# Optimization experiments

Measured on AMD Instinct MI355X. Metric: run time of the kernel, lower is better.

## Reference

```python
import jax, jax.numpy as jnp
import numpy as np

D_MODEL = 1024
N_HEADS = 16
HEAD_DIM = D_MODEL // N_HEADS
D_FF = 4 * D_MODEL
LN_EPS = 1e-5


def setup_inputs() -> dict:
    key = jax.random.key(0)
    ks = jax.random.split(key, 12)
    B, T = 16, 512
    s = lambda fan_in: 1.0 / np.sqrt(fan_in)
    inp = {
        'x': jax.random.normal(ks[0], (B, T, D_MODEL), jnp.float32),
        # torch Linear layout: [out_features, in_features]
        'w_qkv': jax.random.normal(ks[1], (3 * D_MODEL, D_MODEL), jnp.float32) * s(D_MODEL),
        'w_proj': jax.random.normal(ks[2], (D_MODEL, D_MODEL), jnp.float32) * s(D_MODEL),
        'w_ff1': jax.random.normal(ks[3], (D_FF, D_MODEL), jnp.float32) * s(D_MODEL),
        'b_ff1': jax.random.normal(ks[4], (D_FF,), jnp.float32) * 0.02,
        'w_ff2': jax.random.normal(ks[5], (D_MODEL, D_FF), jnp.float32) * s(D_FF),
        'b_ff2': jax.random.normal(ks[6], (D_MODEL,), jnp.float32) * 0.02,
        'ln1_g': jnp.ones((D_MODEL,), jnp.float32),
        'ln1_b': jnp.zeros((D_MODEL,), jnp.float32),
        'ln2_g': jnp.ones((D_MODEL,), jnp.float32),
        'ln2_b': jnp.zeros((D_MODEL,), jnp.float32),
    }
    return inp


def _layernorm(x, g, b):
    mu = jnp.mean(x, axis=-1, keepdims=True)
    var = jnp.var(x, axis=-1, keepdims=True)
    return (x - mu) * jax.lax.rsqrt(var + LN_EPS) * g + b


def _block(x, w_qkv, w_proj, w_ff1, b_ff1, w_ff2, b_ff2, ln1_g, ln1_b, ln2_g, ln2_b):
    B, T, _ = x.shape
    a = _layernorm(x, ln1_g, ln1_b)
    qkv = a @ w_qkv.T  # [B,T,3D]
    q, k, v = jnp.split(qkv, 3, axis=-1)
    # [B,H,T,hd]
    rs = lambda t: t.reshape(B, T, N_HEADS, HEAD_DIM).transpose(0, 2, 1, 3)
    q, k, v = rs(q), rs(k), rs(v)
    scale = HEAD_DIM ** -0.5
    att = jnp.einsum('bhqd,bhkd->bhqk', q, k) * scale
    causal = jnp.tril(jnp.ones((T, T), bool))
    att = jnp.where(causal, att, jnp.float32(-10000.0))
    att = jax.nn.softmax(att, axis=-1)
    out = jnp.einsum('bhqk,bhkd->bhqd', att, v)
    out = out.transpose(0, 2, 1, 3).reshape(B, T, D_MODEL)
    x = x + out @ w_proj.T
    f = _layernorm(x, ln2_g, ln2_b)
    f = jax.nn.gelu(f @ w_ff1.T + b_ff1, approximate=False) @ w_ff2.T + b_ff2
    return x + f


def reference(x, w_qkv, w_proj, w_ff1, b_ff1, w_ff2, b_ff2, ln1_g, ln1_b, ln2_g, ln2_b):
    return _block(x, w_qkv, w_proj, w_ff1, b_ff1, w_ff2, b_ff2, ln1_g, ln1_b, ln2_g, ln2_b)
```

## Files before the change

### kernel.cpp

```cpp
#include <hip/hip_runtime.h>
#include <stdint.h>

typedef __bf16 bf16x8_t __attribute__((ext_vector_type(8)));
typedef float f32x4_t __attribute__((ext_vector_type(4)));
typedef unsigned short ushort8_t __attribute__((ext_vector_type(8)));

#define DEV __device__ __forceinline__

DEV unsigned short f2bf(float f) {
  union { float f; uint32_t u; } v; v.f = f;
  uint32_t r = v.u + 0x7FFFu + ((v.u >> 16) & 1u);
  return (unsigned short)(r >> 16);
}

DEV void gl_lds16(const void* g, void* l) {
  __builtin_amdgcn_global_load_lds(
      (const __attribute__((address_space(1))) void*)g,
      (__attribute__((address_space(3))) void*)l, 16, 0, 0);
}

DEV float gelu_f(float x) {
  const float y = x * 0.7071067811865475f;
  const float ay = fabsf(y);
  const float t = __builtin_amdgcn_rcpf(1.0f + 0.3275911f * ay);
  float p = fmaf(t, 1.061405429f, -1.453152027f);
  p = fmaf(t, p, 1.421413741f);
  p = fmaf(t, p, -0.284496736f);
  p = fmaf(t, p, 0.254829592f);
  p *= t;
  const float e = __expf(-ay * ay);
  float erfv = 1.0f - p * e;
  erfv = copysignf(erfv, y);
  return 0.5f * x * (1.0f + erfv);
}

__global__ __launch_bounds__(256) void cvt_all(const float* __restrict__ w0, unsigned short* __restrict__ o0,
                                               const float* __restrict__ w1, unsigned short* __restrict__ o1,
                                               const float* __restrict__ w2, unsigned short* __restrict__ o2,
                                               const float* __restrict__ w3, unsigned short* __restrict__ o3) {
  int i = blockIdx.x * 256 + threadIdx.x;
  const float* in; unsigned short* outp;
  if (i < 786432) { in = w0; outp = o0; }
  else if (i < 1048576) { in = w1; outp = o1; i -= 786432; }
  else if (i < 2097152) { in = w2; outp = o2; i -= 1048576; }
  else { in = w3; outp = o3; i -= 2097152; }
  float4 v = ((const float4*)in)[i];
  ushort4 o;
  o.x = f2bf(v.x); o.y = f2bf(v.y); o.z = f2bf(v.z); o.w = f2bf(v.w);
  ((ushort4*)outp)[i] = o;
}

__global__ __launch_bounds__(256) void ln_kernel(const float* __restrict__ x,
                                                 const float* __restrict__ g,
                                                 const float* __restrict__ b,
                                                 unsigned short* __restrict__ outp) {
  const int row = blockIdx.x * 4 + (threadIdx.x >> 6);
  const int lane = threadIdx.x & 63;
  const float4* xr = (const float4*)(x + (size_t)row * 1024);
  float4 v[4];
  float s = 0.f, s2 = 0.f;
#pragma unroll
  for (int j = 0; j < 4; ++j) {
    v[j] = xr[j * 64 + lane];
    s += v[j].x + v[j].y + v[j].z + v[j].w;
    s2 += v[j].x * v[j].x + v[j].y * v[j].y + v[j].z * v[j].z + v[j].w * v[j].w;
  }
#pragma unroll
  for (int off = 1; off < 64; off <<= 1) {
    s += __shfl_xor(s, off, 64);
    s2 += __shfl_xor(s2, off, 64);
  }
  const float mu = s * (1.0f / 1024.0f);
  const float var = s2 * (1.0f / 1024.0f) - mu * mu;
  const float rstd = rsqrtf(var + 1e-5f);
  ushort4* orow = (ushort4*)(outp + (size_t)row * 1024);
  const float4* gp = (const float4*)g;
  const float4* bp = (const float4*)b;
#pragma unroll
  for (int j = 0; j < 4; ++j) {
    float4 gv = gp[j * 64 + lane], bv = bp[j * 64 + lane];
    ushort4 o;
    o.x = f2bf((v[j].x - mu) * rstd * gv.x + bv.x);
    o.y = f2bf((v[j].y - mu) * rstd * gv.y + bv.y);
    o.z = f2bf((v[j].z - mu) * rstd * gv.z + bv.z);
    o.w = f2bf((v[j].w - mu) * rstd * gv.w + bv.w);
    orow[j * 64 + lane] = o;
  }
}

template <int MODE>
__global__ __launch_bounds__(256) void gemm_bt(const unsigned short* __restrict__ A,
                                               const unsigned short* __restrict__ B,
                                               float* __restrict__ Cf,
                                               unsigned short* __restrict__ Cb,
                                               const float* __restrict__ bias,
                                               const float* __restrict__ res,
                                               unsigned short* __restrict__ Vt,
                                               int M, int N, int K) {
  __shared__ unsigned short sA[128 * 64];
  __shared__ unsigned short sB[128 * 64];
  const int tid = threadIdx.x;
  const int w = tid >> 6, lane = tid & 63;
  const int kg = lane >> 4, l16 = lane & 15;
  const int wm = (w & 1) * 64, wn = (w >> 1) * 64;
  const int rowBase = blockIdx.y * 128, colBase = blockIdx.x * 128;

  const int sr = tid >> 3;
  const int scc = ((tid & 7) ^ (sr & 7)) * 8;
  const unsigned short* gA = A + (size_t)(rowBase + sr) * K + scc;
  const unsigned short* gB = B + (size_t)(colBase + sr) * K + scc;
  unsigned short* lA = sA + tid * 8;
  unsigned short* lB = sB + tid * 8;

  f32x4_t acc[4][4];
#pragma unroll
  for (int mi = 0; mi < 4; ++mi)
#pragma unroll
    for (int ni = 0; ni < 4; ++ni) acc[mi][ni] = (f32x4_t)0.0f;

  const unsigned short* pA[2][4];
  const unsigned short* pB[2][4];
#pragma unroll
  for (int kd = 0; kd < 2; ++kd)
#pragma unroll
    for (int i = 0; i < 4; ++i) {
      const int kc = kd * 4 + kg;
      pA[kd][i] = sA + (wm + i * 16 + l16) * 64 + ((kc ^ (l16 & 7)) * 8);
      pB[kd][i] = sB + (wn + i * 16 + l16) * 64 + ((kc ^ (l16 & 7)) * 8);
    }

  const int nk = K >> 6;
  for (int kt = 0; kt < nk; ++kt) {
    __syncthreads();
#pragma unroll
    for (int i = 0; i < 4; ++i) {
      gl_lds16(gA + (size_t)(32 * i) * K, lA + 2048 * i);
      gl_lds16(gB + (size_t)(32 * i) * K, lB + 2048 * i);
    }
    gA += 64; gB += 64;
    __syncthreads();
#pragma unroll
    for (int kd = 0; kd < 2; ++kd) {
      bf16x8_t a[4], b[4];
#pragma unroll
      for (int i = 0; i < 4; ++i) a[i] = *(const bf16x8_t*)pA[kd][i];
#pragma unroll
      for (int i = 0; i < 4; ++i) b[i] = *(const bf16x8_t*)pB[kd][i];
#pragma unroll
      for (int mi = 0; mi < 4; ++mi)
#pragma unroll
        for (int ni = 0; ni < 4; ++ni)
          acc[mi][ni] = __builtin_amdgcn_mfma_f32_16x16x32_bf16(a[mi], b[ni], acc[mi][ni], 0, 0, 0);
    }
  }

#pragma unroll
  for (int mi = 0; mi < 4; ++mi) {
#pragma unroll
    for (int ni = 0; ni < 4; ++ni) {
      const int col = colBase + wn + ni * 16 + l16;
      if (MODE == 0 && colBase >= 2048) {
        const int c2 = col - 2048;
        const int hh = c2 >> 6, dd = c2 & 63;
        const int rw = rowBase + wm + mi * 16 + kg * 4;
        ushort4 pk;
        pk.x = f2bf(acc[mi][ni][0]);
        pk.y = f2bf(acc[mi][ni][1]);
        pk.z = f2bf(acc[mi][ni][2]);
        pk.w = f2bf(acc[mi][ni][3]);
        *(ushort4*)(Vt + (((size_t)(rw >> 9) * 16 + hh) * 64 + dd) * 512 + (rw & 511)) = pk;
        continue;
      }
      float bv = 0.f;
      if (MODE == 2 || MODE == 3) bv = bias[col];
#pragma unroll
      for (int r = 0; r < 4; ++r) {
        const int row = rowBase + wm + mi * 16 + kg * 4 + r;
        const size_t idx = (size_t)row * N + col;
        float v = acc[mi][ni][r];
        if (MODE == 0) {
          Cb[idx] = f2bf(v);
        } else if (MODE == 1) {
          Cf[idx] = v + res[idx];
        } else if (MODE == 2) {
          Cb[idx] = f2bf(gelu_f(v + bv));
        } else {
          Cf[idx] = v + bv + res[idx];
        }
      }
    }
  }
}

__global__ __launch_bounds__(256) void attn_kernel(const unsigned short* __restrict__ qkv,
                                                   const unsigned short* __restrict__ Vt,
                                                   unsigned short* __restrict__ outp) {
  constexpr int D3 = 3072;
  __shared__ unsigned short sQ[128 * 64];
  __shared__ unsigned short sK[64 * 64];
  __shared__ unsigned short sVt[64 * 64];
  __shared__ unsigned short sP[128 * 72];
  const int tid = threadIdx.x;
  const int w = tid >> 6, lane = tid & 63;
  const int kg = lane >> 4, l16 = lane & 15;
  const int qi = blockIdx.x, h = blockIdx.y, bb = blockIdx.z;
  const int t0 = qi * 128;
  const size_t base = (size_t)bb * 512 * D3 + h * 64;

  const int sr = tid >> 3;
  const int sc = ((tid & 7) ^ (sr & 7)) * 8;

  {
    const unsigned short* g = qkv + base + (size_t)(t0 + sr) * D3 + sc;
    unsigned short* l = sQ + tid * 8;
#pragma unroll
    for (int i = 0; i < 4; ++i) gl_lds16(g + (size_t)32 * i * D3, l + 2048 * i);
  }

  const unsigned short* gVbase = Vt + ((size_t)(bb * 16 + h) * 64 + sr) * 512 + sc;

  const int wm = w * 32;
  f32x4_t o[2][4];
  float m_i[2][4], l_i[2][4];
#pragma unroll
  for (int mi = 0; mi < 2; ++mi)
#pragma unroll
    for (int r = 0; r < 4; ++r) { m_i[mi][r] = -1e30f; l_i[mi][r] = 0.f; }
#pragma unroll
  for (int mi = 0; mi < 2; ++mi)
#pragma unroll
    for (int di = 0; di < 4; ++di) o[mi][di] = (f32x4_t)0.0f;

  const int nkt = (qi + 1) * 2;
  for (int kt = 0; kt < nkt; ++kt) {
    const int k0 = kt * 64;
    __syncthreads();
    {
      const unsigned short* g = qkv + base + 1024 + (size_t)(k0 + sr) * D3 + sc;
      unsigned short* l = sK + tid * 8;
      gl_lds16(g, l);
      gl_lds16(g + (size_t)32 * D3, l + 2048);
    }
    {
      const unsigned short* g = gVbase + k0;
      unsigned short* l = sVt + tid * 8;
      gl_lds16(g, l);
      gl_lds16(g + (size_t)32 * 512, l + 2048);
    }
    __syncthreads();

    const bool active = (k0 <= t0 + wm + 31);
    if (active) {
      f32x4_t s[2][4];
#pragma unroll
      for (int mi = 0; mi < 2; ++mi)
#pragma unroll
        for (int ni = 0; ni < 4; ++ni) s[mi][ni] = (f32x4_t)0.0f;
#pragma unroll
      for (int kd = 0; kd < 2; ++kd) {
        bf16x8_t aq[2], bk[4];
#pragma unroll
        for (int mi = 0; mi < 2; ++mi) {
          const int rr = wm + mi * 16 + l16;
          aq[mi] = *(const bf16x8_t*)(sQ + rr * 64 + (((kd * 4 + kg) ^ (l16 & 7)) * 8));
        }
#pragma unroll
        for (int ni = 0; ni < 4; ++ni) {
          const int rr = ni * 16 + l16;
          bk[ni] = *(const bf16x8_t*)(sK + rr * 64 + (((kd * 4 + kg) ^ (l16 & 7)) * 8));
        }
#pragma unroll
        for (int mi = 0; mi < 2; ++mi)
#pragma unroll
          for (int ni = 0; ni < 4; ++ni)
            s[mi][ni] = __builtin_amdgcn_mfma_f32_16x16x32_bf16(aq[mi], bk[ni], s[mi][ni], 0, 0, 0);
      }
#pragma unroll
      for (int mi = 0; mi < 2; ++mi) {
#pragma unroll
        for (int r = 0; r < 4; ++r) {
          const int q = t0 + wm + mi * 16 + kg * 4 + r;
          float mx = -1e30f;
#pragma unroll
          for (int ni = 0; ni < 4; ++ni) {
            const int kk = k0 + ni * 16 + l16;
            float v = s[mi][ni][r] * 0.125f;
            v = (kk <= q) ? v : -10000.0f;
            s[mi][ni][r] = v;
            mx = fmaxf(mx, v);
          }
#pragma unroll
          for (int off = 1; off < 16; off <<= 1) mx = fmaxf(mx, __shfl_xor(mx, off, 64));
          const float mo = m_i[mi][r];
          const float mn = fmaxf(mo, mx);
          const float alpha = __expf(mo - mn);
          float ps = 0.f;
#pragma unroll
          for (int ni = 0; ni < 4; ++ni) {
            float p = __expf(s[mi][ni][r] - mn);
            s[mi][ni][r] = p;
            ps += p;
          }
#pragma unroll
          for (int off = 1; off < 16; off <<= 1) ps += __shfl_xor(ps, off, 64);
          l_i[mi][r] = l_i[mi][r] * alpha + ps;
          m_i[mi][r] = mn;
#pragma unroll
          for (int di = 0; di < 4; ++di) o[mi][di][r] *= alpha;
          const int prow = wm + mi * 16 + kg * 4 + r;
#pragma unroll
          for (int ni = 0; ni < 4; ++ni)
            sP[prow * 72 + ni * 16 + l16] = f2bf(s[mi][ni][r]);
        }
      }
#pragma unroll
      for (int kd = 0; kd < 2; ++kd) {
        bf16x8_t ap[2], bv[4];
#pragma unroll
        for (int mi = 0; mi < 2; ++mi)
          ap[mi] = *(const bf16x8_t*)(sP + (wm + mi * 16 + l16) * 72 + kd * 32 + kg * 8);
#pragma unroll
        for (int di = 0; di < 4; ++di) {
          const int dd = di * 16 + l16;
          bv[di] = *(const bf16x8_t*)(sVt + dd * 64 + (((kd * 4 + kg) ^ (l16 & 7)) * 8));
        }
#pragma unroll
        for (int mi = 0; mi < 2; ++mi)
#pragma unroll
          for (int di = 0; di < 4; ++di)
            o[mi][di] = __builtin_amdgcn_mfma_f32_16x16x32_bf16(ap[mi], bv[di], o[mi][di], 0, 0, 0);
      }
    }
  }

#pragma unroll
  for (int mi = 0; mi < 2; ++mi) {
#pragma unroll
    for (int r = 0; r < 4; ++r) {
      const float inv = 1.0f / l_i[mi][r];
      const int row = t0 + wm + mi * 16 + kg * 4 + r;
      const size_t ob = ((size_t)bb * 512 + row) * 1024 + h * 64;
#pragma unroll
      for (int di = 0; di < 4; ++di)
        outp[ob + di * 16 + l16] = f2bf(o[mi][di][r] * inv);
    }
  }
}

extern "C" void kernel_launch(void* const* d_in, const int* in_sizes, int n_in,
                              void* d_out, int out_size, void* d_ws, size_t ws_size,
                              hipStream_t stream) {
  const float* x      = (const float*)d_in[0];
  const float* w_qkv  = (const float*)d_in[1];
  const float* w_proj = (const float*)d_in[2];
  const float* w_ff1  = (const float*)d_in[3];
  const float* b_ff1  = (const float*)d_in[4];
  const float* w_ff2  = (const float*)d_in[5];
  const float* b_ff2  = (const float*)d_in[6];
  const float* ln1_g  = (const float*)d_in[7];
  const float* ln1_b  = (const float*)d_in[8];
  const float* ln2_g  = (const float*)d_in[9];
  const float* ln2_b  = (const float*)d_in[10];
  float* out = (float*)d_out;
  char* ws = (char*)d_ws;

  unsigned short* wqkv_b  = (unsigned short*)(ws + 0);
  unsigned short* wproj_b = (unsigned short*)(ws + 6291456);
  unsigned short* wff1_b  = (unsigned short*)(ws + 8388608);
  unsigned short* wff2_b  = (unsigned short*)(ws + 16777216);
  unsigned short* a_b     = (unsigned short*)(ws + 25165824);
  float*          x2_f    = (float*)(ws + 41943040);
  unsigned short* vt_b    = (unsigned short*)(ws + 41943040);
  unsigned short* qkv_b   = (unsigned short*)(ws + 75497472);
  unsigned short* attn_b  = (unsigned short*)(ws + 125829120);
  unsigned short* h_b     = qkv_b;

  cvt_all<<<12288, 256, 0, stream>>>(w_qkv, wqkv_b, w_proj, wproj_b, w_ff1, wff1_b, w_ff2, wff2_b);

  ln_kernel<<<2048, 256, 0, stream>>>(x, ln1_g, ln1_b, a_b);
  gemm_bt<0><<<dim3(24, 64), 256, 0, stream>>>(a_b, wqkv_b, nullptr, qkv_b, nullptr, nullptr, vt_b, 8192, 3072, 1024);
  attn_kernel<<<dim3(4, 16, 16), 256, 0, stream>>>(qkv_b, vt_b, attn_b);
  gemm_bt<1><<<dim3(8, 64), 256, 0, stream>>>(attn_b, wproj_b, x2_f, nullptr, nullptr, x, nullptr, 8192, 1024, 1024);
  ln_kernel<<<2048, 256, 0, stream>>>(x2_f, ln2_g, ln2_b, a_b);
  gemm_bt<2><<<dim3(32, 64), 256, 0, stream>>>(a_b, wff1_b, nullptr, h_b, b_ff1, nullptr, nullptr, 8192, 4096, 1024);
  gemm_bt<3><<<dim3(8, 64), 256, 0, stream>>>(h_b, wff2_b, out, nullptr, b_ff2, x2_f, nullptr, 8192, 1024, 4096);
}
```

Measured before the change: 497.0 us.

## Double-buffer GEMM LDS tiles with K=32 steps and grouped block rasterization

```diff
diff --git a/kernel.cpp b/kernel.cpp
--- a/kernel.cpp
+++ b/kernel.cpp
@@ -97,20 +97,25 @@
                                                const float* __restrict__ res,
                                                unsigned short* __restrict__ Vt,
                                                int M, int N, int K) {
-  __shared__ unsigned short sA[128 * 64];
-  __shared__ unsigned short sB[128 * 64];
+  __shared__ unsigned short sA[2][128 * 32];
+  __shared__ unsigned short sB[2][128 * 32];
   const int tid = threadIdx.x;
   const int w = tid >> 6, lane = tid & 63;
   const int kg = lane >> 4, l16 = lane & 15;
   const int wm = (w & 1) * 64, wn = (w >> 1) * 64;
-  const int rowBase = blockIdx.y * 128, colBase = blockIdx.x * 128;
-
-  const int sr = tid >> 3;
-  const int scc = ((tid & 7) ^ (sr & 7)) * 8;
-  const unsigned short* gA = A + (size_t)(rowBase + sr) * K + scc;
-  const unsigned short* gB = B + (size_t)(colBase + sr) * K + scc;
-  unsigned short* lA = sA + tid * 8;
-  unsigned short* lB = sB + tid * 8;
+
+  const int gx = gridDim.x;
+  const int cid = blockIdx.y * gx + blockIdx.x;
+  const int span = gx * 8;
+  const int grp = cid / span;
+  const int loc = cid - grp * span;
+  const int rowBase = (grp * 8 + (loc & 7)) * 128;
+  const int colBase = (loc >> 3) * 128;
+
+  const int sr = tid >> 2;
+  const int gc = ((tid & 3) ^ ((sr >> 1) & 3)) * 8;
+  const unsigned short* gA = A + (size_t)(rowBase + sr) * K + gc;
+  const unsigned short* gB = B + (size_t)(colBase + sr) * K + gc;
 
   f32x4_t acc[4][4];
 #pragma unroll
@@ -118,40 +123,42 @@
 #pragma unroll
     for (int ni = 0; ni < 4; ++ni) acc[mi][ni] = (f32x4_t)0.0f;
 
-  const unsigned short* pA[2][4];
-  const unsigned short* pB[2][4];
-#pragma unroll
-  for (int kd = 0; kd < 2; ++kd)
-#pragma unroll
-    for (int i = 0; i < 4; ++i) {
-      const int kc = kd * 4 + kg;
-      pA[kd][i] = sA + (wm + i * 16 + l16) * 64 + ((kc ^ (l16 & 7)) * 8);
-      pB[kd][i] = sB + (wn + i * 16 + l16) * 64 + ((kc ^ (l16 & 7)) * 8);
-    }
-
-  const int nk = K >> 6;
+  int offA[4], offB[4];
+  const int pc = (kg ^ ((l16 >> 1) & 3)) * 8;
+#pragma unroll
+  for (int i = 0; i < 4; ++i) {
+    offA[i] = (wm + i * 16 + l16) * 32 + pc;
+    offB[i] = (wn + i * 16 + l16) * 32 + pc;
+  }
+
+  gl_lds16(gA, &sA[0][tid * 8]);
+  gl_lds16(gA + (size_t)64 * K, &sA[0][2048 + tid * 8]);
+  gl_lds16(gB, &sB[0][tid * 8]);
+  gl_lds16(gB + (size_t)64 * K, &sB[0][2048 + tid * 8]);
+  gA += 32; gB += 32;
+
+  const int nk = K >> 5;
   for (int kt = 0; kt < nk; ++kt) {
     __syncthreads();
-#pragma unroll
-    for (int i = 0; i < 4; ++i) {
-      gl_lds16(gA + (size_t)(32 * i) * K, lA + 2048 * i);
-      gl_lds16(gB + (size_t)(32 * i) * K, lB + 2048 * i);
-    }
-    gA += 64; gB += 64;
-    __syncthreads();
-#pragma unroll
-    for (int kd = 0; kd < 2; ++kd) {
-      bf16x8_t a[4], b[4];
-#pragma unroll
-      for (int i = 0; i < 4; ++i) a[i] = *(const bf16x8_t*)pA[kd][i];
-#pragma unroll
-      for (int i = 0; i < 4; ++i) b[i] = *(const bf16x8_t*)pB[kd][i];
-#pragma unroll
-      for (int mi = 0; mi < 4; ++mi)
-#pragma unroll
-        for (int ni = 0; ni < 4; ++ni)
-          acc[mi][ni] = __builtin_amdgcn_mfma_f32_16x16x32_bf16(a[mi], b[ni], acc[mi][ni], 0, 0, 0);
-    }
+    if (kt + 1 < nk) {
+      const int nb = (kt + 1) & 1;
+      gl_lds16(gA, &sA[nb][tid * 8]);
+      gl_lds16(gA + (size_t)64 * K, &sA[nb][2048 + tid * 8]);
+      gl_lds16(gB, &sB[nb][tid * 8]);
+      gl_lds16(gB + (size_t)64 * K, &sB[nb][2048 + tid * 8]);
+      gA += 32; gB += 32;
+    }
+    const int bo = (kt & 1) * (128 * 32);
+    bf16x8_t a[4], b[4];
+#pragma unroll
+    for (int i = 0; i < 4; ++i) a[i] = *(const bf16x8_t*)(&sA[0][0] + bo + offA[i]);
+#pragma unroll
+    for (int i = 0; i < 4; ++i) b[i] = *(const bf16x8_t*)(&sB[0][0] + bo + offB[i]);
+#pragma unroll
+    for (int mi = 0; mi < 4; ++mi)
+#pragma unroll
+      for (int ni = 0; ni < 4; ++ni)
+        acc[mi][ni] = __builtin_amdgcn_mfma_f32_16x16x32_bf16(a[mi], b[ni], acc[mi][ni], 0, 0, 0);
   }
 
 #pragma unroll
```

After: 477.0 us. -4.0%, faster.
